# Kernel tuning notes

Hardware: AMD Instinct MI355X
Metric: run time of the kernel (lower is better)

## Reference

```python
import jax, jax.numpy as jnp
import numpy as np

B, T, D, H = 4, 1024, 1024, 16


def setup_inputs() -> dict:
    key = jax.random.key(0)
    ks = jax.random.split(key, 8)
    s = 0.02
    return {
        "query": jax.random.normal(ks[0], (B, T, D), jnp.float32),
        "key": jax.random.normal(ks[1], (B, T, D), jnp.float32),
        "values": jax.random.normal(ks[2], (B, T, D), jnp.float32),
        "Wq": jax.random.normal(ks[3], (D, D), jnp.float32) * s,
        "bq": jnp.zeros((D,), jnp.float32),
        "Wv": jax.random.normal(ks[4], (D, D), jnp.float32) * s,
        "bv": jnp.zeros((D,), jnp.float32),
        "Wo": jax.random.normal(ks[5], (D, D), jnp.float32) * s,
        "bo": jnp.zeros((D,), jnp.float32),
        "gammas": jax.random.normal(ks[6], (H,), jnp.float32) * 0.1,
        "ln_g": jnp.ones((D,), jnp.float32),
        "ln_b": jnp.zeros((D,), jnp.float32),
    }


def _layer(query, key, values, Wq, bq, Wv, bv, Wo, bo, gammas, ln_g, ln_b):
    b, t, d = query.shape
    h = gammas.shape[0]
    dk = d // h

    def proj(x, W, bias):  # torch Linear: x @ W.T + b, then split heads -> (b,h,t,dk)
        y = jnp.einsum('btd,ed->bte', x, W) + bias
        return y.reshape(b, t, h, dk).transpose(0, 2, 1, 3)

    q = proj(query, Wq, bq)
    k = proj(key, Wq, bq)   # kq_same=True
    v = proj(values, Wv, bv)

    scores = jnp.einsum('bhqd,bhkd->bhqk', q, k) / np.float32(np.sqrt(dk))
    idx = jnp.arange(t)
    pos = jnp.abs(idx[:, None] - idx[None, :]).astype(scores.dtype)  # |i-j|, (t,t)
    mask = idx[:, None] > idx[None, :]  # strict lower tril (peek_cur=False)
    neg = jnp.asarray(-1e32, scores.dtype)

    # gamma time-effect (computed without grad in original)
    s_ = jax.nn.softmax(jnp.where(mask, scores, neg), axis=-1)
    distcum = jnp.cumsum(s_, axis=-1)
    disttotal = jnp.sum(s_, axis=-1, keepdims=True)
    dist = jnp.sqrt(jnp.clip((disttotal - distcum) * pos, 0.0, None))
    dist = jax.lax.stop_gradient(dist)
    gamma_eff = -jnp.abs(gammas)[None, :, None, None]  # (1,h,1,1)
    total_effect = jnp.clip(jnp.exp(dist * gamma_eff), 1e-5, 1e5)
    scores = scores * total_effect

    p = jax.nn.softmax(jnp.where(mask, scores, neg), axis=-1)
    p = jnp.where(mask, p, 0.0)
    # maxout rescale (maxout=True since peek_cur=False)
    scale = jnp.minimum(1.0 / jnp.max(p, axis=-1, keepdims=True), 5.0)
    p = p * scale

    out = jnp.einsum('bhqk,bhkd->bhqd', p, v)
    concat = out.transpose(0, 2, 1, 3).reshape(b, t, d)
    attn_out = jnp.einsum('btd,ed->bte', concat, Wo) + bo

    x = query + attn_out  # residual (dropout is identity in eval)
    mu = jnp.mean(x, axis=-1, keepdims=True)
    var = jnp.var(x, axis=-1, keepdims=True)
    return (x - mu) / jnp.sqrt(var + 1e-5) * ln_g + ln_b


def reference(query, key, values, Wq, bq, Wv, bv, Wo, bo, gammas, ln_g, ln_b):
    return _layer(query, key, values, Wq, bq, Wv, bv, Wo, bo, gammas, ln_g, ln_b)
```

## Files before the change

### kernel.cpp

```cpp
#include <hip/hip_runtime.h>
#include <hip/hip_bf16.h>
#include <stdint.h>


typedef unsigned short ushort_t;
typedef __attribute__((ext_vector_type(8))) short short8;
typedef __attribute__((ext_vector_type(8))) unsigned short u16x8;
typedef __attribute__((ext_vector_type(4))) float f32x4;
typedef __attribute__((ext_vector_type(4))) unsigned short u16x4;

#define GLB_CAST(p) ((const __attribute__((address_space(1))) void*)(p))
#define LDS_CAST(p) ((__attribute__((address_space(3))) void*)(p))

#if __has_builtin(__builtin_amdgcn_exp2f)
#define EXP2F(x) __builtin_amdgcn_exp2f(x)
#else
#define EXP2F(x) exp2f(x)
#endif

#define LOG2E 1.44269504f

__device__ __forceinline__ float b2f(ushort_t u) {
  union { unsigned int i; float f; } x; x.i = ((unsigned int)u) << 16; return x.f;
}
__device__ __forceinline__ ushort_t f2b(float f) {
  __hip_bfloat16 h = __float2bfloat16(f);
  return *reinterpret_cast<ushort_t*>(&h);
}
__device__ __forceinline__ float wave_max(float v) {
  #pragma unroll
  for (int d = 32; d > 0; d >>= 1) v = fmaxf(v, __shfl_xor(v, d));
  return v;
}
__device__ __forceinline__ float wave_sum(float v) {
  #pragma unroll
  for (int d = 32; d > 0; d >>= 1) v += __shfl_xor(v, d);
  return v;
}

__global__ void conv6_f32_bf16(const float* __restrict__ s0, const float* __restrict__ s1,
                               const float* __restrict__ s2, const float* __restrict__ s3,
                               const float* __restrict__ s4, const float* __restrict__ s5,
                               ushort_t* __restrict__ d0, ushort_t* __restrict__ d1,
                               ushort_t* __restrict__ d2, ushort_t* __restrict__ d3,
                               ushort_t* __restrict__ d4, ushort_t* __restrict__ d5,
                               int n4tok, int n4w) {
  const int y = blockIdx.y;
  const float* srcs[6] = {s0, s1, s2, s3, s4, s5};
  ushort_t*    dsts[6] = {d0, d1, d2, d3, d4, d5};
  const int n4 = (y < 3) ? n4tok : n4w;
  int i = blockIdx.x * blockDim.x + threadIdx.x;
  if (i < n4) {
    const float4 v = reinterpret_cast<const float4*>(srcs[y])[i];
    u16x4 o;
    o[0] = f2b(v.x); o[1] = f2b(v.y); o[2] = f2b(v.z); o[3] = f2b(v.w);
    reinterpret_cast<u16x4*>(dsts[y])[i] = o;
  }
}

__device__ __forceinline__ void gemm_core(const ushort_t* __restrict__ A,
                                          const ushort_t* __restrict__ Bt,
                                          int m0, int n0,
                                          ushort_t* As, ushort_t* Bs,
                                          f32x4 (&acc)[4][4]) {
  const int tid = threadIdx.x, lane = tid & 63;
  const int wid = tid >> 6;
  const int wr = (wid >> 1) * 64, wc = (wid & 1) * 64;
  for (int k0 = 0; k0 < 1024; k0 += 32) {
    #pragma unroll
    for (int it = 0; it < 2; ++it) {
      const int idx = tid * 8 + it * 2048;
      const int r = idx >> 5, kk = idx & 31;
      __builtin_amdgcn_global_load_lds(GLB_CAST(&A[(size_t)(m0 + r) * 1024 + k0 + kk]),
                                       LDS_CAST(&As[idx]), 16, 0, 0);
      __builtin_amdgcn_global_load_lds(GLB_CAST(&Bt[(size_t)(n0 + r) * 1024 + k0 + kk]),
                                       LDS_CAST(&Bs[idx]), 16, 0, 0);
    }
    __syncthreads();
    short8 af[4], bfv[4];
    #pragma unroll
    for (int m = 0; m < 4; ++m)
      af[m] = *reinterpret_cast<const short8*>(&As[(wr + m * 16 + (lane & 15)) * 32 + (lane >> 4) * 8]);
    #pragma unroll
    for (int n = 0; n < 4; ++n)
      bfv[n] = *reinterpret_cast<const short8*>(&Bs[(wc + n * 16 + (lane & 15)) * 32 + (lane >> 4) * 8]);
    #pragma unroll
    for (int m = 0; m < 4; ++m)
      #pragma unroll
      for (int n = 0; n < 4; ++n)
        acc[m][n] = __builtin_amdgcn_mfma_f32_16x16x32_bf16(af[m], bfv[n], acc[m][n], 0, 0, 0);
    __syncthreads();
  }
}

__global__ __launch_bounds__(256) void gemm_proj(
    const ushort_t* __restrict__ qb, const ushort_t* __restrict__ kb, const ushort_t* __restrict__ vb,
    const ushort_t* __restrict__ Wqb, const ushort_t* __restrict__ Wvb,
    const float* __restrict__ bq, const float* __restrict__ bvv,
    ushort_t* __restrict__ Qh, ushort_t* __restrict__ Kh, ushort_t* __restrict__ Vt) {
  __shared__ ushort_t As[128 * 32], Bs[128 * 32];
  const ushort_t* A; const ushort_t* Bt; const float* bias;
  if (blockIdx.z == 0)      { A = qb; Bt = Wqb; bias = bq;  }
  else if (blockIdx.z == 1) { A = kb; Bt = Wqb; bias = bq;  }
  else                      { A = vb; Bt = Wvb; bias = bvv; }
  const int m0 = blockIdx.y * 128, n0 = blockIdx.x * 128;
  f32x4 zero = {0.f, 0.f, 0.f, 0.f};
  f32x4 acc[4][4];
  #pragma unroll
  for (int m = 0; m < 4; ++m)
    #pragma unroll
    for (int n = 0; n < 4; ++n) acc[m][n] = zero;
  gemm_core(A, Bt, m0, n0, As, Bs, acc);
  const int lane = threadIdx.x & 63, wid = threadIdx.x >> 6;
  const int wr = (wid >> 1) * 64, wc = (wid & 1) * 64;
  if (blockIdx.z == 2) {
    #pragma unroll
    for (int m = 0; m < 4; ++m)
      #pragma unroll
      for (int n = 0; n < 4; ++n) {
        const int rowb = m0 + wr + m * 16 + (lane >> 4) * 4;
        const int col  = n0 + wc + n * 16 + (lane & 15);
        u16x4 pk;
        #pragma unroll
        for (int r4 = 0; r4 < 4; ++r4) pk[r4] = f2b(acc[m][n][r4] + bias[col]);
        const int bi = rowb >> 10, t = rowb & 1023;
        *reinterpret_cast<u16x4*>(
            &Vt[((size_t)(bi * 16 + (col >> 6)) * 64 + (col & 63)) * 1024 + t]) = pk;
      }
  } else {
    ushort_t* dst = (blockIdx.z == 0) ? Qh : Kh;
    #pragma unroll
    for (int m = 0; m < 4; ++m)
      #pragma unroll
      for (int n = 0; n < 4; ++n)
        #pragma unroll
        for (int r4 = 0; r4 < 4; ++r4) {
          const int row = m0 + wr + m * 16 + (lane >> 4) * 4 + r4;
          const int col = n0 + wc + n * 16 + (lane & 15);
          const float v = acc[m][n][r4] + bias[col];
          const int bi = row >> 10, t = row & 1023, h = col >> 6, dd = col & 63;
          dst[((size_t)(bi * 16 + h) * 1024 + t) * 64 + dd] = f2b(v);
        }
  }
}

__global__ __launch_bounds__(256) void gemm_out(
    const ushort_t* __restrict__ A, const ushort_t* __restrict__ Bt,
    const float* __restrict__ bias, const float* __restrict__ resid,
    float* __restrict__ dstF) {
  __shared__ ushort_t As[128 * 32], Bs[128 * 32];
  const int m0 = blockIdx.y * 128, n0 = blockIdx.x * 128;
  f32x4 zero = {0.f, 0.f, 0.f, 0.f};
  f32x4 acc[4][4];
  #pragma unroll
  for (int m = 0; m < 4; ++m)
    #pragma unroll
    for (int n = 0; n < 4; ++n) acc[m][n] = zero;
  gemm_core(A, Bt, m0, n0, As, Bs, acc);
  const int lane = threadIdx.x & 63, wid = threadIdx.x >> 6;
  const int wr = (wid >> 1) * 64, wc = (wid & 1) * 64;
  #pragma unroll
  for (int m = 0; m < 4; ++m)
    #pragma unroll
    for (int n = 0; n < 4; ++n)
      #pragma unroll
      for (int r4 = 0; r4 < 4; ++r4) {
        const int row = m0 + wr + m * 16 + (lane >> 4) * 4 + r4;
        const int col = n0 + wc + n * 16 + (lane & 15);
        const size_t o = (size_t)row * 1024 + col;
        dstF[o] = acc[m][n][r4] + bias[col] + resid[o];
      }
}

template<int CH>
__device__ __forceinline__ void phase_b(ushort_t* __restrict__ Sb, const int i0,
                                        const int w, const int lane, const float gamx) {
  const int c0 = CH * lane;
  int idxA = 0, idxB = 0;
  if constexpr (CH == 16) {
    const int ca = 2 * lane, cb = 2 * lane + 1;
    idxA = (ca ^ ((ca >> 3) & 7)) << 3;
    idxB = (cb ^ ((cb >> 3) & 7)) << 3;
  } else {
    const int c = c0 >> 3;
    idxA = ((c ^ ((c >> 3) & 7)) << 3) + (c0 & 7);
  }
  for (int rr = 0; rr < 4; ++rr) {
    const int r = w * 4 + rr;
    const int i = i0 + r;
    ushort_t* __restrict__ Row = &Sb[r * 1032];
    if (i == 0) {
      #pragma unroll
      for (int e = 0; e < CH; ++e) {
        if constexpr (CH == 16) Row[(e < 8) ? (idxA + e) : (idxB + e - 8)] = 0;
        else                    Row[idxA + e] = 0;
      }
      continue;
    }
    float s[CH];
    if constexpr (CH == 16) {
      const u16x8 ra = *reinterpret_cast<const u16x8*>(&Row[idxA]);
      const u16x8 rb = *reinterpret_cast<const u16x8*>(&Row[idxB]);
      #pragma unroll
      for (int e = 0; e < 8; ++e) { s[e] = b2f(ra[e]); s[8 + e] = b2f(rb[e]); }
    } else if constexpr (CH == 8) {
      const u16x8 ra = *reinterpret_cast<const u16x8*>(&Row[idxA]);
      #pragma unroll
      for (int e = 0; e < 8; ++e) s[e] = b2f(ra[e]);
    } else if constexpr (CH == 4) {
      const u16x4 ra = *reinterpret_cast<const u16x4*>(&Row[idxA]);
      #pragma unroll
      for (int e = 0; e < 4; ++e) s[e] = b2f(ra[e]);
    } else if constexpr (CH == 2) {
      s[0] = b2f(Row[idxA]); s[1] = b2f(Row[idxA + 1]);
    } else {
      s[0] = b2f(Row[idxA]);
    }
    const int nact = min(max(i - c0, 0), CH);
    #pragma unroll
    for (int e = 0; e < CH; ++e)
      s[e] = (e < nact) ? s[e] * LOG2E : -__builtin_inff();
    float m1 = s[0];
    #pragma unroll
    for (int e = 1; e < CH; ++e) m1 = fmaxf(m1, s[e]);
    m1 = wave_max(m1);
    float ev[CH], tl[CH];
    float run = 0.f;
    #pragma unroll
    for (int e = CH - 1; e >= 0; --e) {
      ev[e] = EXP2F(s[e] - m1);
      tl[e] = run; run += ev[e];
    }
    float v = run;
    #pragma unroll
    for (int d = 1; d < 64; d <<= 1) {
      const float t = __shfl_down(v, d);
      v += (lane + d < 64) ? t : 0.f;
    }
    const float Z1 = __shfl(v, 0);
    const float excl = v - run;
    const float g2 = -gamx * sqrtf(1.f / Z1);
    const float posb = (float)(i - c0);
    float m2 = -__builtin_inff();
    #pragma unroll
    for (int e = 0; e < CH; ++e) {
      const float t = fmaxf((tl[e] + excl) * (posb - (float)e), 0.f);
      const float eff = fmaxf(EXP2F(g2 * sqrtf(t)), 1e-5f);
      s[e] *= eff;
      m2 = fmaxf(m2, s[e]);
    }
    m2 = wave_max(m2);
    float z2 = 0.f;
    #pragma unroll
    for (int e = 0; e < CH; ++e) { ev[e] = EXP2F(s[e] - m2); z2 += ev[e]; }
    const float Z2 = wave_sum(z2);
    const float sc = fminf(Z2, 5.f) / Z2;
    if constexpr (CH == 16) {
      u16x8 oa, ob;
      #pragma unroll
      for (int e = 0; e < 8; ++e) { oa[e] = f2b(ev[e] * sc); ob[e] = f2b(ev[8 + e] * sc); }
      *reinterpret_cast<u16x8*>(&Row[idxA]) = oa;
      *reinterpret_cast<u16x8*>(&Row[idxB]) = ob;
    } else if constexpr (CH == 8) {
      u16x8 oa;
      #pragma unroll
      for (int e = 0; e < 8; ++e) oa[e] = f2b(ev[e] * sc);
      *reinterpret_cast<u16x8*>(&Row[idxA]) = oa;
    } else if constexpr (CH == 4) {
      u16x4 oa;
      #pragma unroll
      for (int e = 0; e < 4; ++e) oa[e] = f2b(ev[e] * sc);
      *reinterpret_cast<u16x4*>(&Row[idxA]) = oa;
    } else if constexpr (CH == 2) {
      Row[idxA] = f2b(ev[0] * sc); Row[idxA + 1] = f2b(ev[1] * sc);
    } else {
      Row[idxA] = f2b(ev[0] * sc);
    }
  }
}

__global__ __launch_bounds__(256, 4) void attn_kernel(
    const ushort_t* __restrict__ Qh, const ushort_t* __restrict__ Kh,
    const ushort_t* __restrict__ Vt, const float* __restrict__ gammas,
    ushort_t* __restrict__ concat) {
  __shared__ __align__(16) ushort_t Sb[16 * 1032];
  __shared__ __align__(16) ushort_t Qs[16 * 72];
  const int tid = threadIdx.x, lane = tid & 63, w = tid >> 6;
  const int bh = blockIdx.y, bi = bh >> 4, h = bh & 15;
  const int i0 = blockIdx.x * 16;
  const size_t base = (size_t)bh * (1024 * 64);

  {
    const int r = tid >> 4, d = (tid & 15) * 4;
    *reinterpret_cast<u16x4*>(&Qs[r * 72 + d]) =
        *reinterpret_cast<const u16x4*>(&Qh[base + (size_t)(i0 + r) * 64 + d]);
  }
  __syncthreads();

  const int upper = i0 + 16;
  for (int nt = 0; nt < 16; ++nt) {
    const int colbase = (nt * 4 + w) * 16;
    if (colbase >= upper) break;
    f32x4 acc = {0.f, 0.f, 0.f, 0.f};
    #pragma unroll
    for (int kt = 0; kt < 2; ++kt) {
      const short8 a = *reinterpret_cast<const short8*>(
          &Qs[(lane & 15) * 72 + kt * 32 + (lane >> 4) * 8]);
      const short8 bb = *reinterpret_cast<const short8*>(
          &Kh[base + (size_t)(colbase + (lane & 15)) * 64 + kt * 32 + (lane >> 4) * 8]);
      acc = __builtin_amdgcn_mfma_f32_16x16x32_bf16(a, bb, acc, 0, 0, 0);
    }
    const int j = colbase + (lane & 15);
    const int cq = (j >> 3) ^ ((j >> 6) & 7);
    const int ub = cq * 8 + (j & 7);
    #pragma unroll
    for (int r4 = 0; r4 < 4; ++r4) {
      const int rf = (lane >> 4) * 4 + r4;
      Sb[rf * 1032 + ub] = f2b(acc[r4] * 0.125f);
    }
  }
  __syncthreads();

  const float gamx = fabsf(gammas[h]) * LOG2E;
  const int chp = (upper + 63) >> 6;
  if (chp == 1)      phase_b<1>(Sb, i0, w, lane, gamx);
  else if (chp == 2) phase_b<2>(Sb, i0, w, lane, gamx);
  else if (chp <= 4) phase_b<4>(Sb, i0, w, lane, gamx);
  else if (chp <= 8) phase_b<8>(Sb, i0, w, lane, gamx);
  else               phase_b<16>(Sb, i0, w, lane, gamx);
  __syncthreads();

  {
    const int d0 = w * 16;
    const int arow = lane & 15;
    const ushort_t* Prow = &Sb[arow * 1032];
    const ushort_t* Vrow = Vt + base + (size_t)(d0 + arow) * 1024;
    const int kmax = (upper + 31) & ~31;
    f32x4 acc = {0.f, 0.f, 0.f, 0.f};
    for (int k0 = 0; k0 < kmax; k0 += 32) {
      const int c = (k0 >> 3) + (lane >> 4);
      const int cq = c ^ ((c >> 3) & 7);
      const short8 a = *reinterpret_cast<const short8*>(&Prow[cq * 8]);
      const short8 bb = *reinterpret_cast<const short8*>(&Vrow[k0 + (lane >> 4) * 8]);
      acc = __builtin_amdgcn_mfma_f32_16x16x32_bf16(a, bb, acc, 0, 0, 0);
    }
    #pragma unroll
    for (int r4 = 0; r4 < 4; ++r4) {
      const int row = (lane >> 4) * 4 + r4;
      const int i = i0 + row;
      concat[((size_t)(bi * 1024 + i)) * 1024 + h * 64 + d0 + arow] = f2b(acc[r4]);
    }
  }
}

__global__ __launch_bounds__(256) void ln_kernel(const float* __restrict__ x,
                                                 const float* __restrict__ g,
                                                 const float* __restrict__ bb,
                                                 float* __restrict__ out) {
  const int row = blockIdx.x, tid = threadIdx.x, lane = tid & 63, w = tid >> 6;
  const float4 v = reinterpret_cast<const float4*>(x + (size_t)row * 1024)[tid];
  float s = v.x + v.y + v.z + v.w;
  float q = v.x * v.x + v.y * v.y + v.z * v.z + v.w * v.w;
  s = wave_sum(s); q = wave_sum(q);
  __shared__ float ps[4], pq[4];
  if (lane == 0) { ps[w] = s; pq[w] = q; }
  __syncthreads();
  const float ts = ps[0] + ps[1] + ps[2] + ps[3];
  const float tq = pq[0] + pq[1] + pq[2] + pq[3];
  const float mu = ts * (1.f / 1024.f);
  const float inv = rsqrtf(tq * (1.f / 1024.f) - mu * mu + 1e-5f);
  const float4 gv = reinterpret_cast<const float4*>(g)[tid];
  const float4 bv = reinterpret_cast<const float4*>(bb)[tid];
  float4 o;
  o.x = (v.x - mu) * inv * gv.x + bv.x;
  o.y = (v.y - mu) * inv * gv.y + bv.y;
  o.z = (v.z - mu) * inv * gv.z + bv.z;
  o.w = (v.w - mu) * inv * gv.w + bv.w;
  reinterpret_cast<float4*>(out + (size_t)row * 1024)[tid] = o;
}

extern "C" void kernel_launch(void* const* d_in, const int* in_sizes, int n_in,
                              void* d_out, int out_size, void* d_ws, size_t ws_size,
                              hipStream_t stream) {
  (void)in_sizes; (void)n_in; (void)out_size; (void)ws_size;
  const float* query  = (const float*)d_in[0];
  const float* key    = (const float*)d_in[1];
  const float* values = (const float*)d_in[2];
  const float* Wq     = (const float*)d_in[3];
  const float* bq     = (const float*)d_in[4];
  const float* Wv     = (const float*)d_in[5];
  const float* bv     = (const float*)d_in[6];
  const float* Wo     = (const float*)d_in[7];
  const float* bo     = (const float*)d_in[8];
  const float* gammas = (const float*)d_in[9];
  const float* ln_g   = (const float*)d_in[10];
  const float* ln_b   = (const float*)d_in[11];
  float* out = (float*)d_out;

  const size_t NT = 4096ull * 1024;
  const size_t NW = 1024ull * 1024;
  char* p = (char*)d_ws;
  ushort_t* qb  = (ushort_t*)p; p += NT * 2;
  ushort_t* kb  = (ushort_t*)p; p += NT * 2;
  ushort_t* vb  = (ushort_t*)p; p += NT * 2;
  ushort_t* Wqb = (ushort_t*)p; p += NW * 2;
  ushort_t* Wvb = (ushort_t*)p; p += NW * 2;
  ushort_t* Wob = (ushort_t*)p; p += NW * 2;
  ushort_t* Qh  = (ushort_t*)p; p += NT * 2;
  ushort_t* Kh  = (ushort_t*)p; p += NT * 2;
  ushort_t* Vt  = (ushort_t*)p; p += NT * 2;
  ushort_t* concat = vb;
  float*    xbuf   = (float*)qb;

  conv6_f32_bf16<<<dim3(4096, 6), 256, 0, stream>>>(
      query, key, values, Wq, Wv, Wo, qb, kb, vb, Wqb, Wvb, Wob,
      (int)(NT / 4), (int)(NW / 4));

  gemm_proj<<<dim3(8, 32, 3), 256, 0, stream>>>(qb, kb, vb, Wqb, Wvb, bq, bv, Qh, Kh, Vt);
  attn_kernel<<<dim3(64, 64), 256, 0, stream>>>(Qh, Kh, Vt, gammas, concat);
  gemm_out<<<dim3(8, 32), 256, 0, stream>>>(concat, Wob, bo, query, xbuf);
  ln_kernel<<<4096, 256, 0, stream>>>(xbuf, ln_g, ln_b, out);
}
```

Before: 202.5 us.

## Drop softmax max-subtraction and use 512-thread attention blocks with two rows per wave

```diff
diff --git a/kernel.cpp b/kernel.cpp
--- a/kernel.cpp
+++ b/kernel.cpp
@@ -26,11 +26,6 @@
 __device__ __forceinline__ ushort_t f2b(float f) {
   __hip_bfloat16 h = __float2bfloat16(f);
   return *reinterpret_cast<ushort_t*>(&h);
-}
-__device__ __forceinline__ float wave_max(float v) {
-  #pragma unroll
-  for (int d = 32; d > 0; d >>= 1) v = fmaxf(v, __shfl_xor(v, d));
-  return v;
 }
 __device__ __forceinline__ float wave_sum(float v) {
   #pragma unroll
@@ -185,8 +180,9 @@
     const int c = c0 >> 3;
     idxA = ((c ^ ((c >> 3) & 7)) << 3) + (c0 & 7);
   }
-  for (int rr = 0; rr < 4; ++rr) {
-    const int r = w * 4 + rr;
+  #pragma unroll
+  for (int rr = 0; rr < 2; ++rr) {
+    const int r = w * 2 + rr;
     const int i = i0 + r;
     ushort_t* __restrict__ Row = &Sb[r * 1032];
     if (i == 0) {
@@ -220,17 +216,10 @@
     #pragma unroll
     for (int e = 0; e < CH; ++e)
       s[e] = (e < nact) ? s[e] * LOG2E : -__builtin_inff();
-    float m1 = s[0];
-    #pragma unroll
-    for (int e = 1; e < CH; ++e) m1 = fmaxf(m1, s[e]);
-    m1 = wave_max(m1);
-    float ev[CH], tl[CH];
+    float ev[CH];
     float run = 0.f;
     #pragma unroll
-    for (int e = CH - 1; e >= 0; --e) {
-      ev[e] = EXP2F(s[e] - m1);
-      tl[e] = run; run += ev[e];
-    }
+    for (int e = 0; e < CH; ++e) { ev[e] = EXP2F(s[e]); run += ev[e]; }
     float v = run;
     #pragma unroll
     for (int d = 1; d < 64; d <<= 1) {
@@ -239,22 +228,29 @@
     }
     const float Z1 = __shfl(v, 0);
     const float excl = v - run;
-    const float g2 = -gamx * sqrtf(1.f / Z1);
+    const float g2 = -gamx * rsqrtf(Z1);
     const float posb = (float)(i - c0);
-    float m2 = -__builtin_inff();
-    #pragma unroll
-    for (int e = 0; e < CH; ++e) {
-      const float t = fmaxf((tl[e] + excl) * (posb - (float)e), 0.f);
+    float run2 = excl;
+    #pragma unroll
+    for (int e = CH - 1; e >= 0; --e) {
+      const float t = fmaxf(run2 * (posb - (float)e), 0.f);
+      run2 += ev[e];
       const float eff = fmaxf(EXP2F(g2 * sqrtf(t)), 1e-5f);
       s[e] *= eff;
-      m2 = fmaxf(m2, s[e]);
-    }
-    m2 = wave_max(m2);
-    float z2 = 0.f;
-    #pragma unroll
-    for (int e = 0; e < CH; ++e) { ev[e] = EXP2F(s[e] - m2); z2 += ev[e]; }
-    const float Z2 = wave_sum(z2);
-    const float sc = fminf(Z2, 5.f) / Z2;
+    }
+    float z2 = 0.f, mm = 0.f;
+    #pragma unroll
+    for (int e = 0; e < CH; ++e) {
+      ev[e] = EXP2F(s[e]);
+      z2 += ev[e];
+      mm = fmaxf(mm, ev[e]);
+    }
+    #pragma unroll
+    for (int d = 32; d > 0; d >>= 1) {
+      z2 += __shfl_xor(z2, d);
+      mm = fmaxf(mm, __shfl_xor(mm, d));
+    }
+    const float sc = fminf(1.f / mm, 5.f / z2);
     if constexpr (CH == 16) {
       u16x8 oa, ob;
       #pragma unroll
@@ -279,7 +275,7 @@
   }
 }
 
-__global__ __launch_bounds__(256, 4) void attn_kernel(
+__global__ __launch_bounds__(512, 6) void attn_kernel(
     const ushort_t* __restrict__ Qh, const ushort_t* __restrict__ Kh,
     const ushort_t* __restrict__ Vt, const float* __restrict__ gammas,
     ushort_t* __restrict__ concat) {
@@ -290,7 +286,7 @@
   const int i0 = blockIdx.x * 16;
   const size_t base = (size_t)bh * (1024 * 64);
 
-  {
+  if (tid < 256) {
     const int r = tid >> 4, d = (tid & 15) * 4;
     *reinterpret_cast<u16x4*>(&Qs[r * 72 + d]) =
         *reinterpret_cast<const u16x4*>(&Qh[base + (size_t)(i0 + r) * 64 + d]);
@@ -298,8 +294,8 @@
   __syncthreads();
 
   const int upper = i0 + 16;
-  for (int nt = 0; nt < 16; ++nt) {
-    const int colbase = (nt * 4 + w) * 16;
+  for (int nt = 0; nt < 8; ++nt) {
+    const int colbase = (nt * 8 + w) * 16;
     if (colbase >= upper) break;
     f32x4 acc = {0.f, 0.f, 0.f, 0.f};
     #pragma unroll
@@ -330,7 +326,7 @@
   else               phase_b<16>(Sb, i0, w, lane, gamx);
   __syncthreads();
 
-  {
+  if (w < 4) {
     const int d0 = w * 16;
     const int arow = lane & 15;
     const ushort_t* Prow = &Sb[arow * 1032];
@@ -417,7 +413,7 @@
       (int)(NT / 4), (int)(NW / 4));
 
   gemm_proj<<<dim3(8, 32, 3), 256, 0, stream>>>(qb, kb, vb, Wqb, Wvb, bq, bv, Qh, Kh, Vt);
-  attn_kernel<<<dim3(64, 64), 256, 0, stream>>>(Qh, Kh, Vt, gammas, concat);
+  attn_kernel<<<dim3(64, 64), 512, 0, stream>>>(Qh, Kh, Vt, gammas, concat);
   gemm_out<<<dim3(8, 32), 256, 0, stream>>>(concat, Wob, bo, query, xbuf);
   ln_kernel<<<4096, 256, 0, stream>>>(xbuf, ln_g, ln_b, out);
 }
```

Result: faster. 190.7 us (-5.8%).
